# Optimization experiments

Hardware: AMD Instinct MI355X
Metric: run time of the kernel (lower is better)

The kernel has to match this reference:

```python
import jax, jax.numpy as jnp
import numpy as np
import math

DENOM = 32.0

# e3nn scalar_activation normalizes the activation to unit second moment under N(0,1).
# Compute the gelu normalization constant by Gauss-Hermite quadrature.
_zs, _ws = np.polynomial.hermite_e.hermegauss(64)
_g = 0.5 * _zs * (1.0 + np.array([math.erf(z / math.sqrt(2.0)) for z in _zs]))
C_GELU = float(1.0 / math.sqrt((_ws * _g * _g).sum() / math.sqrt(2.0 * math.pi)))


def _spherical_harmonics(r):
    # r: [E,3] unit vectors. Component-normalized real SH for l=1,2,3.
    x, y, z = r[..., 0], r[..., 1], r[..., 2]
    s3, s5, s15 = math.sqrt(3.0), math.sqrt(5.0), math.sqrt(15.0)
    s7, s105 = math.sqrt(7.0), math.sqrt(105.0)
    s35_8, s21_8 = math.sqrt(35.0 / 8.0), math.sqrt(21.0 / 8.0)
    Y1 = s3 * r                                                     # [E,3]
    Y2 = jnp.stack([s15 * x * y, s15 * y * z, 0.5 * s5 * (3 * z * z - 1),
                    s15 * x * z, 0.5 * s15 * (x * x - y * y)], -1)   # [E,5]
    Y3 = jnp.stack([s35_8 * y * (3 * x * x - y * y), s105 * x * y * z,
                    s21_8 * y * (5 * z * z - 1), 0.5 * s7 * z * (5 * z * z - 3),
                    s21_8 * x * (5 * z * z - 1), 0.5 * s105 * z * (x * x - y * y),
                    s35_8 * x * (x * x - 3 * y * y)], -1)            # [E,7]
    return [Y1, Y2, Y3]


def setup_inputs() -> dict:
    key = jax.random.key(0)
    k = jax.random.split(key, 7)
    N, E, MUL, TMUL = 32768, 1048576, 16, 32
    return {
        "x": jax.random.normal(k[0], (N, MUL), jnp.float32),
        "positions": jax.random.normal(k[1], (N, 3), jnp.float32),
        "W_pre": jax.random.normal(k[2], (4, MUL, TMUL), jnp.float32),
        "W_post": jax.random.normal(k[3], (4, TMUL, TMUL), jnp.float32),
        "W_shortcut": jax.random.normal(k[4], (MUL, TMUL), jnp.float32),
        "senders": jax.random.randint(k[5], (E,), 0, N, jnp.int32),
        "receivers": jax.random.randint(k[6], (E,), 0, N, jnp.int32),
    }


def reference(x, positions, W_pre, W_post, W_shortcut, senders, receivers):
    N, mul = x.shape
    tmul = W_pre.shape[-1]
    # --- edge update: sh of relative positions, tensor product with sender scalars ---
    rvec = positions[receivers] - positions[senders]                 # [E,3]
    n = jnp.linalg.norm(rvec, axis=-1, keepdims=True)
    rhat = rvec / jnp.where(n == 0, 1.0, n)
    Ys = _spherical_harmonics(rhat)
    s = x[senders]                                                   # [E,mul] (0e)
    # --- aggregate edge features at receivers (segment sum) ---
    agg = [jax.ops.segment_sum(s, receivers, num_segments=N)]        # 0e block
    for Y in Ys:
        e = (s[:, :, None] * Y[:, None, :]).reshape(s.shape[0], -1)  # 0e x l -> l
        agg.append(jax.ops.segment_sum(e, receivers, num_segments=N).reshape(N, mul, Y.shape[-1]))
    # --- node update: linear_pre -> scalar act -> linear_post, plus shortcut ---
    inv_in = 1.0 / math.sqrt(mul)
    inv_mid = 1.0 / math.sqrt(tmul)
    out = []
    for l in range(4):
        a = agg[l] / DENOM
        if l == 0:
            p = (a @ W_pre[0]) * inv_in
            p = C_GELU * jax.nn.gelu(p, approximate=False)           # act on 0e scalars only
            q = (p @ W_post[0]) * inv_mid
            q = q + (x @ W_shortcut) * inv_in                        # shortcut: only 0e path exists
            out.append(q)
        else:
            p = jnp.einsum('nui,uv->nvi', a, W_pre[l]) * inv_in
            q = jnp.einsum('nvi,vw->nwi', p, W_post[l]) * inv_mid
            out.append(q.reshape(N, -1))
    return jnp.concatenate(out, axis=-1)                              # [N, tmul*16]
```

## Files before the change

### kernel.cpp

```cpp
#include <hip/hip_runtime.h>
#include <math.h>

#define NN 32768
#define EN 1048576
#define NBIN 256
#define BINCAP 8192
#define TILE 4096

#define C_GELU_F 1.5335262f

__global__ __launch_bounds__(512) void bin_k(const int* __restrict__ snd,
                                             const int* __restrict__ rcv,
                                             int* __restrict__ bin_cur,
                                             unsigned* __restrict__ binbuf) {
    __shared__ unsigned cnt[NBIN];
    __shared__ unsigned excl[NBIN];
    __shared__ unsigned cur2[NBIN];
    __shared__ unsigned gbase[NBIN];
    __shared__ unsigned stage[TILE];
    int t = threadIdx.x;
    int tile = blockIdx.x * TILE;
    if (t < NBIN) { cnt[t] = 0; cur2[t] = 0; }
    __syncthreads();

    unsigned w[TILE / 512];
#pragma unroll
    for (int i = 0; i < TILE / 512; ++i) {
        int e = tile + i * 512 + t;
        unsigned r = (unsigned)rcv[e], s = (unsigned)snd[e];
        w[i] = (r << 15) | s;
        atomicAdd(&cnt[w[i] >> 22], 1u);
    }
    __syncthreads();

    unsigned my = (t < NBIN) ? cnt[t] : 0u;
    if (t < NBIN) excl[t] = my;
    __syncthreads();
    for (int d = 1; d < NBIN; d <<= 1) {
        unsigned v = (t < NBIN && t >= d) ? excl[t - d] : 0u;
        __syncthreads();
        if (t < NBIN) excl[t] += v;
        __syncthreads();
    }
    if (t < NBIN) {
        unsigned myexcl = excl[t] - my;
        gbase[t] = atomicAdd((unsigned*)&bin_cur[t], my);
        excl[t] = myexcl;
    }
    __syncthreads();

#pragma unroll
    for (int i = 0; i < TILE / 512; ++i) {
        unsigned b = w[i] >> 22;
        unsigned p = excl[b] + atomicAdd(&cur2[b], 1u);
        stage[p] = w[i];
    }
    __syncthreads();

    for (int p = t; p < TILE; p += 512) {
        unsigned ww = stage[p];
        unsigned b = ww >> 22;
        unsigned idx = gbase[b] + ((unsigned)p - excl[b]);
        if (idx < BINCAP) binbuf[b * BINCAP + idx] = ww;
    }
}

__global__ __launch_bounds__(256) void scan_k(const int* __restrict__ bin_cur,
                                              int* __restrict__ bin_start) {
    __shared__ unsigned sc[NBIN];
    int t = threadIdx.x;
    unsigned my = (unsigned)bin_cur[t];
    sc[t] = my;
    __syncthreads();
    for (int d = 1; d < NBIN; d <<= 1) {
        unsigned v = (t >= d) ? sc[t - d] : 0u;
        __syncthreads();
        sc[t] += v;
        __syncthreads();
    }
    bin_start[t] = (int)(sc[t] - my);
}

__global__ __launch_bounds__(1024) void csr_k(const int* __restrict__ bin_cur,
                                              const int* __restrict__ bin_start,
                                              const unsigned* __restrict__ binbuf,
                                              int* __restrict__ row_ptr,
                                              int* __restrict__ edge_csr) {
    __shared__ unsigned cnt[128];
    __shared__ unsigned excl[128];
    __shared__ unsigned cur2[128];
    int b = blockIdx.x;
    int t = threadIdx.x;
    int M = bin_cur[b]; M = M > BINCAP ? BINCAP : M;
    int base = bin_start[b];
    if (t < 128) { cnt[t] = 0; cur2[t] = 0; }
    __syncthreads();

    const unsigned* bb = binbuf + b * BINCAP;
    for (int i = t; i < M; i += 1024)
        atomicAdd(&cnt[(bb[i] >> 15) & 127], 1u);
    __syncthreads();

    if (t < 128) excl[t] = cnt[t];
    __syncthreads();
    for (int d = 1; d < 128; d <<= 1) {
        unsigned v = (t >= d && t < 128) ? excl[t - d] : 0u;
        __syncthreads();
        if (t < 128) excl[t] += v;
        __syncthreads();
    }
    if (t < 128) {
        unsigned e = excl[t] - cnt[t];
        excl[t] = e;
        row_ptr[(b << 7) + t] = base + (int)e;
        if (b == NBIN - 1 && t == 127) row_ptr[NN] = base + (int)(e + cnt[127]);
    }
    __syncthreads();

    for (int i = t; i < M; i += 1024) {
        unsigned ww = bb[i];
        unsigned r7 = (ww >> 15) & 127;
        unsigned dst = excl[r7] + atomicAdd(&cur2[r7], 1u);
        edge_csr[base + dst] = (int)(ww & 0x7FFF);
    }
}

__global__ __launch_bounds__(256) void pos_k(const float* __restrict__ pos,
                                             float4* __restrict__ posw) {
    int n = blockIdx.x * 256 + threadIdx.x;
    posw[n] = make_float4(pos[3*n], pos[3*n+1], pos[3*n+2], 0.f);
}

#define GROUPS 32
#define BLK 512
#define YST 20
#define GST (16*YST + 8)

__global__ __launch_bounds__(512, 4) void fused_k(const float* __restrict__ x,
                                                  const float4* __restrict__ posw,
                                                  const int* __restrict__ row_ptr,
                                                  const int* __restrict__ edge_csr,
                                                  const float* __restrict__ Wpre,
                                                  const float* __restrict__ Wpost,
                                                  const float* __restrict__ Wsc,
                                                  float* __restrict__ out) {
    __shared__ float sPre[4*516];
    __shared__ float sPost[4*1028];
    __shared__ float sSc[512];
    __shared__ float sY[GROUPS * GST];

    int t = threadIdx.x;
    for (int idx = t; idx < 2048; idx += BLK)
        sPre[(idx >> 9)*516 + (idx & 511)] = Wpre[idx];
    for (int idx = t; idx < 4096; idx += BLK)
        sPost[(idx >> 10)*1028 + (idx & 1023)] = Wpost[idx];
    sSc[t] = Wsc[t];

    int g = t >> 4;
    int j = t & 15;
    int n = blockIdx.x * GROUPS + g;
    int beg = row_ptr[n], end = row_ptr[n + 1];
    int cnt = end - beg;
    float4 rp = posw[n];
    float* yg = sY + g * GST;

    const float s3   = 1.7320508075688772f;
    const float s5   = 2.2360679774997896f;
    const float s15  = 3.8729833462074170f;
    const float s7   = 2.6457513110645907f;
    const float s105 = 10.246950765959598f;
    const float s35_8 = 2.0916500663351889f;
    const float s21_8 = 1.6201851746019651f;

    float acc[16];
#pragma unroll
    for (int u = 0; u < 16; ++u) acc[u] = 0.f;

    int nch = (cnt + 15) >> 4;
    for (int c = 0; c < nch; ++c) {
        int rem = cnt - (c << 4); rem = rem > 16 ? 16 : rem;

        int k = (c << 4) + j;
        int ki = k < cnt ? k : cnt - 1;
        int sE = edge_csr[beg + ki];
        float4 sp = posw[sE];
        float vx = rp.x - sp.x, vy = rp.y - sp.y, vz = rp.z - sp.z;
        float n2 = vx*vx + vy*vy + vz*vz;
        float inv;
        if (n2 > 0.f) {
            inv = rsqrtf(n2);
            inv = inv * (1.5f - 0.5f * n2 * inv * inv);
        } else inv = 0.f;
        float X = vx*inv, Y = vy*inv, Z = vz*inv;
        float XX = X*X, YY = Y*Y, ZZ = Z*Z;

        float* yr = yg + j * YST;
        ((float4*)yr)[0] = make_float4(1.f, s3*X, s3*Y, s3*Z);
        ((float4*)yr)[1] = make_float4(s15*X*Y, s15*Y*Z,
                                       0.5f*s5*(3.f*ZZ - 1.f), s15*X*Z);
        ((float4*)yr)[2] = make_float4(0.5f*s15*(XX - YY),
                                       s35_8*Y*(3.f*XX - YY),
                                       s105*X*Y*Z,
                                       s21_8*Y*(5.f*ZZ - 1.f));
        ((float4*)yr)[3] = make_float4(0.5f*s7*Z*(5.f*ZZ - 3.f),
                                       s21_8*X*(5.f*ZZ - 1.f),
                                       0.5f*s105*Z*(XX - YY),
                                       s35_8*X*(XX - 3.f*YY));

#pragma unroll 4
        for (int e = 0; e < rem; ++e) {
            int se = __shfl(sE, (t & 48) + e, 64);
            float y = yg[e * YST + j];
            const float4* xp = (const float4*)(x + (se << 4));
            float4 a0 = xp[0], a1 = xp[1], a2 = xp[2], a3 = xp[3];
            acc[0]  += a0.x * y;  acc[1]  += a0.y * y;
            acc[2]  += a0.z * y;  acc[3]  += a0.w * y;
            acc[4]  += a1.x * y;  acc[5]  += a1.y * y;
            acc[6]  += a1.z * y;  acc[7]  += a1.w * y;
            acc[8]  += a2.x * y;  acc[9]  += a2.y * y;
            acc[10] += a2.z * y;  acc[11] += a2.w * y;
            acc[12] += a3.x * y;  acc[13] += a3.y * y;
            acc[14] += a3.z * y;  acc[15] += a3.w * y;
        }
    }
    __syncthreads();

    int l, i, offl, deg;
    if (j == 0)      { l = 0; i = 0;     offl = 0;   deg = 1; }
    else if (j < 4)  { l = 1; i = j - 1; offl = 32;  deg = 3; }
    else if (j < 9)  { l = 2; i = j - 4; offl = 128; deg = 5; }
    else             { l = 3; i = j - 9; offl = 288; deg = 7; }

    const float c1 = 0.0078125f;
    const float c2 = 0.17677669529663687f;

    float p[32];
#pragma unroll
    for (int v = 0; v < 32; ++v) p[v] = 0.f;
    const float* wp = sPre + l * 516;
#pragma unroll
    for (int uu = 0; uu < 16; ++uu) {
        float a = acc[uu];
        const float4* w4 = (const float4*)(wp + (uu << 5));
#pragma unroll
        for (int vq = 0; vq < 8; ++vq) {
            float4 w = w4[vq];
            p[4*vq+0] += a * w.x;
            p[4*vq+1] += a * w.y;
            p[4*vq+2] += a * w.z;
            p[4*vq+3] += a * w.w;
        }
    }
#pragma unroll
    for (int v = 0; v < 32; ++v) p[v] *= c1;

    if (j == 0) {
#pragma unroll
        for (int v = 0; v < 32; ++v) {
            float pv = p[v];
            p[v] = C_GELU_F * 0.5f * pv * (1.f + erff(pv * 0.7071067811865476f));
        }
    }

    float q[32];
#pragma unroll
    for (int w = 0; w < 32; ++w) q[w] = 0.f;
    const float* wq = sPost + l * 1028;
#pragma unroll
    for (int v = 0; v < 32; ++v) {
        float pv = p[v];
        const float4* w4 = (const float4*)(wq + (v << 5));
#pragma unroll
        for (int wd = 0; wd < 8; ++wd) {
            float4 w = w4[wd];
            q[4*wd+0] += pv * w.x;
            q[4*wd+1] += pv * w.y;
            q[4*wd+2] += pv * w.z;
            q[4*wd+3] += pv * w.w;
        }
    }
#pragma unroll
    for (int w = 0; w < 32; ++w) q[w] *= c2;

    if (j == 0) {
        const float* xp = x + (n << 4);
#pragma unroll
        for (int uu = 0; uu < 16; ++uu) {
            float xv = 0.25f * xp[uu];
            const float4* w4 = (const float4*)(sSc + (uu << 5));
#pragma unroll
            for (int wd = 0; wd < 8; ++wd) {
                float4 w = w4[wd];
                q[4*wd+0] += xv * w.x;
                q[4*wd+1] += xv * w.y;
                q[4*wd+2] += xv * w.z;
                q[4*wd+3] += xv * w.w;
            }
        }
    }

    float* op = out + (n << 9) + offl + i;
#pragma unroll
    for (int w = 0; w < 32; ++w) op[w * deg] = q[w];
}

extern "C" void kernel_launch(void* const* d_in, const int* in_sizes, int n_in,
                              void* d_out, int out_size, void* d_ws, size_t ws_size,
                              hipStream_t stream) {
    const float* x     = (const float*)d_in[0];
    const float* pos   = (const float*)d_in[1];
    const float* Wpre  = (const float*)d_in[2];
    const float* Wpost = (const float*)d_in[3];
    const float* Wsc   = (const float*)d_in[4];
    const int*   snd   = (const int*)d_in[5];
    const int*   rcv   = (const int*)d_in[6];
    float* out = (float*)d_out;

    char* ws = (char*)d_ws;
    int*      bin_cur   = (int*)(ws);
    int*      bin_start = (int*)(ws + 1024);
    int*      row_ptr   = (int*)(ws + 2048);
    float4*   posw      = (float4*)(ws + 0x30000);
    int*      edge_csr  = (int*)(ws + 0xB0000);
    unsigned* binbuf    = (unsigned*)(ws + 0x500000);

    hipMemsetAsync(bin_cur, 0, NBIN * sizeof(int), stream);
    bin_k<<<EN / TILE, 512, 0, stream>>>(snd, rcv, bin_cur, binbuf);
    scan_k<<<1, 256, 0, stream>>>(bin_cur, bin_start);
    csr_k<<<NBIN, 1024, 0, stream>>>(bin_cur, bin_start, binbuf, row_ptr, edge_csr);
    pos_k<<<NN / 256, 256, 0, stream>>>(pos, posw);
    fused_k<<<NN / GROUPS, BLK, 0, stream>>>(x, posw, row_ptr, edge_csr,
                                             Wpre, Wpost, Wsc, out);
}
```

Measured before the change: 197.9 us.

## Pack sender positions into CSR edge records and shrink fused kernel shared memory

The CSR build kernel now caches bin words in LDS and writes a float4 per edge holding the sender position and index, so the fused kernel no longer does a dependent gather into positions. The separate pos_k kernel is removed. The fused kernel moves to 256-thread blocks with 16 groups and loads the weights into LDS after aggregation, reusing the same buffer as the Y staging area. The inner loop is fully unrolled over 16 edges with masked Y values in place of a variable trip count. The cost is a 16-byte edge record instead of 4 bytes, and wasted gather work on partially filled chunks.

Measured after the change: 201.6 us. No clear change (+1.9%).

```diff
diff --git a/kernel.cpp b/kernel.cpp
--- a/kernel.cpp
+++ b/kernel.cpp
@@ -81,14 +81,16 @@
     bin_start[t] = (int)(sc[t] - my);
 }
 
-__global__ __launch_bounds__(1024) void csr_k(const int* __restrict__ bin_cur,
-                                              const int* __restrict__ bin_start,
-                                              const unsigned* __restrict__ binbuf,
-                                              int* __restrict__ row_ptr,
-                                              int* __restrict__ edge_csr) {
+__global__ __launch_bounds__(1024) void csrfill_k(const int* __restrict__ bin_cur,
+                                                  const int* __restrict__ bin_start,
+                                                  const unsigned* __restrict__ binbuf,
+                                                  const float* __restrict__ pos,
+                                                  int* __restrict__ row_ptr,
+                                                  float4* __restrict__ edata) {
     __shared__ unsigned cnt[128];
     __shared__ unsigned excl[128];
     __shared__ unsigned cur2[128];
+    __shared__ unsigned words[BINCAP];
     int b = blockIdx.x;
     int t = threadIdx.x;
     int M = bin_cur[b]; M = M > BINCAP ? BINCAP : M;
@@ -97,8 +99,11 @@
     __syncthreads();
 
     const unsigned* bb = binbuf + b * BINCAP;
-    for (int i = t; i < M; i += 1024)
-        atomicAdd(&cnt[(bb[i] >> 15) & 127], 1u);
+    for (int i = t; i < M; i += 1024) {
+        unsigned ww = bb[i];
+        words[i] = ww;
+        atomicAdd(&cnt[(ww >> 15) & 127], 1u);
+    }
     __syncthreads();
 
     if (t < 128) excl[t] = cnt[t];
@@ -118,51 +123,39 @@
     __syncthreads();
 
     for (int i = t; i < M; i += 1024) {
-        unsigned ww = bb[i];
+        unsigned ww = words[i];
         unsigned r7 = (ww >> 15) & 127;
         unsigned dst = excl[r7] + atomicAdd(&cur2[r7], 1u);
-        edge_csr[base + dst] = (int)(ww & 0x7FFF);
-    }
-}
-
-__global__ __launch_bounds__(256) void pos_k(const float* __restrict__ pos,
-                                             float4* __restrict__ posw) {
-    int n = blockIdx.x * 256 + threadIdx.x;
-    posw[n] = make_float4(pos[3*n], pos[3*n+1], pos[3*n+2], 0.f);
-}
-
-#define GROUPS 32
-#define BLK 512
-#define YST 20
-#define GST (16*YST + 8)
-
-__global__ __launch_bounds__(512, 4) void fused_k(const float* __restrict__ x,
-                                                  const float4* __restrict__ posw,
+        int s = (int)(ww & 0x7FFF);
+        const float* ps = pos + 3 * s;
+        edata[base + dst] = make_float4(ps[0], ps[1], ps[2], __int_as_float(s));
+    }
+}
+
+#define GROUPS 16
+#define BLK 256
+#define GST 344
+#define SU_FLOATS 6688
+
+__global__ __launch_bounds__(256, 4) void fused_k(const float* __restrict__ x,
+                                                  const float* __restrict__ pos,
                                                   const int* __restrict__ row_ptr,
-                                                  const int* __restrict__ edge_csr,
+                                                  const float4* __restrict__ edata,
                                                   const float* __restrict__ Wpre,
                                                   const float* __restrict__ Wpost,
                                                   const float* __restrict__ Wsc,
                                                   float* __restrict__ out) {
-    __shared__ float sPre[4*516];
-    __shared__ float sPost[4*1028];
-    __shared__ float sSc[512];
-    __shared__ float sY[GROUPS * GST];
+    __shared__ float sU[SU_FLOATS];
 
     int t = threadIdx.x;
-    for (int idx = t; idx < 2048; idx += BLK)
-        sPre[(idx >> 9)*516 + (idx & 511)] = Wpre[idx];
-    for (int idx = t; idx < 4096; idx += BLK)
-        sPost[(idx >> 10)*1028 + (idx & 1023)] = Wpost[idx];
-    sSc[t] = Wsc[t];
-
     int g = t >> 4;
     int j = t & 15;
     int n = blockIdx.x * GROUPS + g;
     int beg = row_ptr[n], end = row_ptr[n + 1];
     int cnt = end - beg;
-    float4 rp = posw[n];
-    float* yg = sY + g * GST;
+    const float* pr = pos + 3 * n;
+    float rpx = pr[0], rpy = pr[1], rpz = pr[2];
+    float* yg = sU + g * GST;
 
     const float s3   = 1.7320508075688772f;
     const float s5   = 2.2360679774997896f;
@@ -178,40 +171,56 @@
 
     int nch = (cnt + 15) >> 4;
     for (int c = 0; c < nch; ++c) {
-        int rem = cnt - (c << 4); rem = rem > 16 ? 16 : rem;
-
         int k = (c << 4) + j;
-        int ki = k < cnt ? k : cnt - 1;
-        int sE = edge_csr[beg + ki];
-        float4 sp = posw[sE];
-        float vx = rp.x - sp.x, vy = rp.y - sp.y, vz = rp.z - sp.z;
+        bool valid = k < cnt;
+        int ki = valid ? k : cnt - 1;
+        float4 rec = edata[beg + ki];
+        int sE = __float_as_int(rec.w);
+        float vx = rpx - rec.x, vy = rpy - rec.y, vz = rpz - rec.z;
         float n2 = vx*vx + vy*vy + vz*vz;
         float inv;
-        if (n2 > 0.f) {
+        if (valid && n2 > 0.f) {
             inv = rsqrtf(n2);
             inv = inv * (1.5f - 0.5f * n2 * inv * inv);
         } else inv = 0.f;
         float X = vx*inv, Y = vy*inv, Z = vz*inv;
         float XX = X*X, YY = Y*Y, ZZ = Z*Z;
-
-        float* yr = yg + j * YST;
-        ((float4*)yr)[0] = make_float4(1.f, s3*X, s3*Y, s3*Z);
-        ((float4*)yr)[1] = make_float4(s15*X*Y, s15*Y*Z,
-                                       0.5f*s5*(3.f*ZZ - 1.f), s15*X*Z);
-        ((float4*)yr)[2] = make_float4(0.5f*s15*(XX - YY),
-                                       s35_8*Y*(3.f*XX - YY),
-                                       s105*X*Y*Z,
-                                       s21_8*Y*(5.f*ZZ - 1.f));
-        ((float4*)yr)[3] = make_float4(0.5f*s7*Z*(5.f*ZZ - 3.f),
-                                       s21_8*X*(5.f*ZZ - 1.f),
-                                       0.5f*s105*Z*(XX - YY),
-                                       s35_8*X*(XX - 3.f*YY));
-
-#pragma unroll 4
-        for (int e = 0; e < rem; ++e) {
-            int se = __shfl(sE, (t & 48) + e, 64);
-            float y = yg[e * YST + j];
-            const float4* xp = (const float4*)(x + (se << 4));
+        float zm = valid ? 1.f : 0.f;
+
+        yg[ 0*20 + j] = zm;
+        yg[ 1*20 + j] = s3*X;
+        yg[ 2*20 + j] = s3*Y;
+        yg[ 3*20 + j] = s3*Z;
+        yg[ 4*20 + j] = s15*X*Y;
+        yg[ 5*20 + j] = s15*Y*Z;
+        yg[ 6*20 + j] = zm * (0.5f*s5*(3.f*ZZ - 1.f));
+        yg[ 7*20 + j] = s15*X*Z;
+        yg[ 8*20 + j] = 0.5f*s15*(XX - YY);
+        yg[ 9*20 + j] = s35_8*Y*(3.f*XX - YY);
+        yg[10*20 + j] = s105*X*Y*Z;
+        yg[11*20 + j] = s21_8*Y*(5.f*ZZ - 1.f);
+        yg[12*20 + j] = 0.5f*s7*Z*(5.f*ZZ - 3.f);
+        yg[13*20 + j] = s21_8*X*(5.f*ZZ - 1.f);
+        yg[14*20 + j] = 0.5f*s105*Z*(XX - YY);
+        yg[15*20 + j] = s35_8*X*(XX - 3.f*YY);
+        ((int*)(yg + 320))[j] = sE;
+
+        const float4* yp = (const float4*)(yg + j * 20);
+        float4 yv0 = yp[0], yv1 = yp[1], yv2 = yp[2], yv3 = yp[3];
+        const int4* sip = (const int4*)(yg + 320);
+        int4 sa0 = sip[0], sa1 = sip[1], sa2 = sip[2], sa3 = sip[3];
+        float yarr[16] = { yv0.x, yv0.y, yv0.z, yv0.w,
+                           yv1.x, yv1.y, yv1.z, yv1.w,
+                           yv2.x, yv2.y, yv2.z, yv2.w,
+                           yv3.x, yv3.y, yv3.z, yv3.w };
+        int sarr[16] = { sa0.x, sa0.y, sa0.z, sa0.w,
+                         sa1.x, sa1.y, sa1.z, sa1.w,
+                         sa2.x, sa2.y, sa2.z, sa2.w,
+                         sa3.x, sa3.y, sa3.z, sa3.w };
+#pragma unroll
+        for (int e = 0; e < 16; ++e) {
+            float y = yarr[e];
+            const float4* xp = (const float4*)(x + (sarr[e] << 4));
             float4 a0 = xp[0], a1 = xp[1], a2 = xp[2], a3 = xp[3];
             acc[0]  += a0.x * y;  acc[1]  += a0.y * y;
             acc[2]  += a0.z * y;  acc[3]  += a0.w * y;
@@ -223,6 +232,17 @@
             acc[14] += a3.z * y;  acc[15] += a3.w * y;
         }
     }
+
+    __syncthreads();
+    float* sPre  = sU;
+    float* sPost = sU + 2064;
+    float* sSc   = sU + 6176;
+    for (int idx = t; idx < 2048; idx += BLK)
+        sPre[(idx >> 9)*516 + (idx & 511)] = Wpre[idx];
+    for (int idx = t; idx < 4096; idx += BLK)
+        sPost[(idx >> 10)*1028 + (idx & 1023)] = Wpost[idx];
+    sSc[t] = Wsc[t];
+    sSc[t + 256] = Wsc[t + 256];
     __syncthreads();
 
     int l, i, offl, deg;
@@ -318,17 +338,16 @@
 
     char* ws = (char*)d_ws;
     int*      bin_cur   = (int*)(ws);
-    int*      bin_start = (int*)(ws + 1024);
-    int*      row_ptr   = (int*)(ws + 2048);
-    float4*   posw      = (float4*)(ws + 0x30000);
-    int*      edge_csr  = (int*)(ws + 0xB0000);
-    unsigned* binbuf    = (unsigned*)(ws + 0x500000);
+    int*      bin_start = (int*)(ws + 0x400);
+    int*      row_ptr   = (int*)(ws + 0x800);
+    unsigned* binbuf    = (unsigned*)(ws + 0x40000);
+    float4*   edata     = (float4*)(ws + 0x900000);
 
     hipMemsetAsync(bin_cur, 0, NBIN * sizeof(int), stream);
     bin_k<<<EN / TILE, 512, 0, stream>>>(snd, rcv, bin_cur, binbuf);
     scan_k<<<1, 256, 0, stream>>>(bin_cur, bin_start);
-    csr_k<<<NBIN, 1024, 0, stream>>>(bin_cur, bin_start, binbuf, row_ptr, edge_csr);
-    pos_k<<<NN / 256, 256, 0, stream>>>(pos, posw);
-    fused_k<<<NN / GROUPS, BLK, 0, stream>>>(x, posw, row_ptr, edge_csr,
+    csrfill_k<<<NBIN, 1024, 0, stream>>>(bin_cur, bin_start, binbuf, pos,
+                                         row_ptr, edata);
+    fused_k<<<NN / GROUPS, BLK, 0, stream>>>(x, pos, row_ptr, edata,
                                              Wpre, Wpost, Wsc, out);
 }
```
